# Kernel optimization log

Hardware: AMD Instinct MI355X
Metric: run time of the kernel (lower is better)

The kernel has to match this reference:

```python
import jax, jax.numpy as jnp
import numpy as np

FEATURE_DIM = 128
NUM_EDGES = 640000
NUM_NODES = 40000


def setup_inputs() -> dict:
    key = jax.random.key(0)
    ks = jax.random.split(key, 10)
    d = FEATURE_DIM
    scale = 1.0 / np.sqrt(d)
    inp = {
        "messages": jax.random.normal(ks[0], (NUM_EDGES, d), dtype=jnp.float32),
        "receivers": jax.random.randint(ks[1], (NUM_EDGES,), 0, NUM_NODES, dtype=jnp.int32),
        "num_segments": NUM_NODES,
        "Wk": jax.random.normal(ks[2], (d, d), dtype=jnp.float32) * scale,
        "bk": jnp.zeros((d,), dtype=jnp.float32),
        "Wv": jax.random.normal(ks[3], (d, d), dtype=jnp.float32) * scale,
        "bv": jnp.zeros((d,), dtype=jnp.float32),
        "Wq": jax.random.normal(ks[4], (d, d), dtype=jnp.float32) * scale,
        "bq": jnp.zeros((d,), dtype=jnp.float32),
        "Wo": jax.random.normal(ks[5], (d, d), dtype=jnp.float32) * scale,
        "bo": jnp.zeros((d,), dtype=jnp.float32),
    }
    return inp


def reference(messages, receivers, num_segments, Wk, bk, Wv, bv, Wq, bq, Wo, bo):
    d = messages.shape[-1]
    # per-edge key/value projections
    keys = messages @ Wk + bk            # [E, d]
    values = messages @ Wv + bv          # [E, d]
    # node-level summed messages -> queries
    summed = jax.ops.segment_sum(messages, receivers, num_segments)  # [N, d]
    queries = summed @ Wq + bq                                       # [N, d]
    # scalar attention score per edge (dot over full feature dim)
    msg_q = queries[receivers]                                       # [E, d]
    scores = jnp.sum(msg_q * keys, axis=-1) / jnp.sqrt(jnp.float32(d))  # [E]
    # segment softmax over edges sharing a receiver
    max_s = jax.ops.segment_max(scores, receivers, num_segments)     # [N]
    exp_s = jnp.exp(scores - max_s[receivers])                       # [E]
    sum_e = jax.ops.segment_sum(exp_s, receivers, num_segments)      # [N]
    attn = exp_s / (sum_e[receivers] + 1e-08)                        # [E]
    # weighted scatter-sum of values, then output projection
    agg = jax.ops.segment_sum(values * attn[:, None], receivers, num_segments)  # [N, d]
    return agg @ Wo + bo
```

## Files before the change

kernel.cpp:

```cpp
#include <hip/hip_runtime.h>

#define D 128
#define RSQRT_D 0.088388347648318440550f
#define NEG_HUGE -3.4e38f
#define NPB 16
#define CAP 512

#define FMA4(acc, s, b) { acc.x += (s)*(b).x; acc.y += (s)*(b).y; acc.z += (s)*(b).z; acc.w += (s)*(b).w; }
#define ADD4(acc, b) { acc.x += (b).x; acc.y += (b).y; acc.z += (b).z; acc.w += (b).w; }
#define MRG4(a) { a.x += __shfl_xor(a.x,32); a.y += __shfl_xor(a.y,32); a.z += __shfl_xor(a.z,32); a.w += __shfl_xor(a.w,32); }
#define Z4 make_float4(0.f,0.f,0.f,0.f)

__global__ __launch_bounds__(256) void prep_kernel(
    const float* __restrict__ Wq, const float* __restrict__ Wk,
    const float* __restrict__ bq, const float* __restrict__ bk,
    const float* __restrict__ Wv, const float* __restrict__ Wo,
    const float* __restrict__ bv,
    float* __restrict__ Wqk, float* __restrict__ bqk,
    float* __restrict__ wqb, float* __restrict__ bqb,
    float* __restrict__ Wvo, float* __restrict__ bvo,
    int* __restrict__ zbase, int zcount) {
    int bid = blockIdx.x, t = threadIdx.x;
    if (bid < 64) {
        int i = bid * 2 + (t >> 7), j = t & 127;
        float a1 = 0.f, a2 = 0.f;
        for (int u = 0; u < D; ++u) {
            a1 += Wq[i * D + u] * Wk[j * D + u];
            a2 += Wv[i * D + u] * Wo[u * D + j];
        }
        Wqk[i * D + j] = a1;
        Wvo[i * D + j] = a2;
    } else if (bid == 64) {
        if (t < D) {
            int j = t;
            float a1 = 0.f, a2 = 0.f, a3 = 0.f;
            for (int u = 0; u < D; ++u) {
                a1 += bq[u] * Wk[j * D + u];
                a2 += Wq[j * D + u] * bk[u];
                a3 += bv[u] * Wo[u * D + j];
            }
            bqk[j] = a1; wqb[j] = a2; bvo[j] = a3;
            if (j == 0) {
                float b = 0.f;
                for (int u = 0; u < D; ++u) b += bq[u] * bk[u];
                *bqb = b;
            }
        }
    } else {
        int idx = (bid - 65) * 256 + t;
        if (idx < zcount) zbase[idx] = 0;
    }
}

__global__ void hist_kernel(const int* __restrict__ recv, int* __restrict__ cnt, int E) {
    int e = blockIdx.x * blockDim.x + threadIdx.x;
    if (e >= E) return;
    atomicAdd(&cnt[recv[e]], 1);
}

__global__ __launch_bounds__(1024) void scan_kernel(const int* __restrict__ cnt,
                                                    int* __restrict__ start, int N) {
    __shared__ int wsum[16];
    __shared__ int chunk_total;
    int t = threadIdx.x;
    int w = t >> 6, lane = t & 63;
    int running = 0;
    const int4* cnt4 = (const int4*)cnt;
    int nIter = (N + 4095) >> 12;
    int4 v = make_int4(0, 0, 0, 0);
    {
        int i = t << 2;
        if (i < N) v = cnt4[i >> 2];
    }
    for (int it = 0; it < nIter; ++it) {
        int4 vn = make_int4(0, 0, 0, 0);
        {
            int i = ((it + 1) << 12) + (t << 2);
            if (it + 1 < nIter && i < N) vn = cnt4[i >> 2];
        }
        int s0 = v.x, s1 = s0 + v.y, s2 = s1 + v.z, s3 = s2 + v.w;
        int x = s3;
#pragma unroll
        for (int off = 1; off < 64; off <<= 1) {
            int y = __shfl_up(x, off);
            if (lane >= off) x += y;
        }
        if (lane == 63) wsum[w] = x;
        __syncthreads();
        if (w == 0 && lane < 16) {
            int s = wsum[lane];
#pragma unroll
            for (int off = 1; off < 16; off <<= 1) {
                int y = __shfl_up(s, off);
                if (lane >= off) s += y;
            }
            wsum[lane] = s;
            if (lane == 15) chunk_total = s;
        }
        __syncthreads();
        int waveoff = (w == 0) ? 0 : wsum[w - 1];
        int tb = running + waveoff + (x - s3);
        int i = (it << 12) + (t << 2);
        if (i < N) ((int4*)start)[i >> 2] = make_int4(tb, tb + s0, tb + s1, tb + s2);
        running += chunk_total;
        __syncthreads();
        v = vn;
    }
    if (t == 0) start[N] = running;
}

__global__ void fill_kernel(const int* __restrict__ recv, const int* __restrict__ start,
                            int* __restrict__ cursor, int* __restrict__ eidx, int E) {
    int e = blockIdx.x * blockDim.x + threadIdx.x;
    if (e >= E) return;
    int r = recv[e];
    int p = atomicAdd(&cursor[r], 1);
    eidx[start[r] + p] = e;
}

__device__ __forceinline__ float hdot32(float4 f, float4 q) {
    float p = f.x * q.x + f.y * q.y + f.z * q.z + f.w * q.w;
    p += __shfl_xor(p, 1); p += __shfl_xor(p, 2); p += __shfl_xor(p, 4);
    p += __shfl_xor(p, 8); p += __shfl_xor(p, 16);
    return p;
}

__global__ __launch_bounds__(256, 4) void mega_kernel(
    const float* __restrict__ msg, const int* __restrict__ eidx,
    const int* __restrict__ start,
    const float* __restrict__ Wqk, const float* __restrict__ bqk,
    const float* __restrict__ wqb, const float* __restrict__ bqbp,
    const float* __restrict__ Wvo, const float* __restrict__ bvo,
    const float* __restrict__ bo,
    float* __restrict__ out, int N) {
    __shared__ float4 sums4[NPB * 32];
    __shared__ float4 qks4[NPB * 32];
    __shared__ int eidx_s[CAP];
    __shared__ float s_s[CAP];
    __shared__ float sat[NPB];

    int t = threadIdx.x;
    int lane = t & 63, w = t >> 6;
    int h = lane >> 5;
    int k = lane & 31;
    int base = blockIdx.x * NPB;
    const float4* msg4 = (const float4*)msg;

    int nendB = min(base + NPB, N);
    int s0B = start[base];
    int cntB = start[nendB] - s0B;
    int cc = min(cntB, CAP);
    for (int i = t; i < cc; i += 256) eidx_s[i] = eidx[s0B + i];

    int n0 = base + w * 4;
    int b0 = start[min(n0 + 0, N)] - s0B;
    int b1 = start[min(n0 + 1, N)] - s0B;
    int b2 = start[min(n0 + 2, N)] - s0B;
    int b3 = start[min(n0 + 3, N)] - s0B;
    int b4 = start[min(n0 + 4, N)] - s0B;

    __syncthreads();

    auto loadrow = [&](int r) -> float4 {
        int rI = min(r, b4 - 1);
        int e = (rI < CAP) ? eidx_s[rI] : eidx[s0B + rI];
        return msg4[(size_t)e * 32 + k];
    };

    float4 a0 = Z4, a1 = Z4, a2 = Z4, a3 = Z4;
    if (b0 < b4) {
        int j = b0;
        float4 F0 = loadrow(j + h), F1 = loadrow(j + h + 2),
               F2 = loadrow(j + h + 4), F3 = loadrow(j + h + 6);
        for (;;) {
            int jn = j + 8;
            bool more = jn < b4;
            float4 G0, G1, G2, G3;
            if (more) {
                G0 = loadrow(jn + h); G1 = loadrow(jn + h + 2);
                G2 = loadrow(jn + h + 4); G3 = loadrow(jn + h + 6);
            }
#pragma unroll
            for (int u = 0; u < 4; ++u) {
                int r = j + h + 2 * u;
                float4 g = (u == 0) ? F0 : (u == 1) ? F1 : (u == 2) ? F2 : F3;
                float mk = (r < b4) ? 1.f : 0.f;
                g.x *= mk; g.y *= mk; g.z *= mk; g.w *= mk;
                if (r < b1)      { ADD4(a0, g); }
                else if (r < b2) { ADD4(a1, g); }
                else if (r < b3) { ADD4(a2, g); }
                else             { ADD4(a3, g); }
            }
            if (!more) break;
            F0 = G0; F1 = G1; F2 = G2; F3 = G3;
            j = jn;
        }
    }
    MRG4(a0); MRG4(a1); MRG4(a2); MRG4(a3);
    if (lane < 32) {
        sums4[(w * 4 + 0) * 32 + k] = a0;
        sums4[(w * 4 + 1) * 32 + k] = a1;
        sums4[(w * 4 + 2) * 32 + k] = a2;
        sums4[(w * 4 + 3) * 32 + k] = a3;
    }
    __syncthreads();

    {
        int c = t & 31, slot = t >> 5;
        const float4* B4 = (const float4*)Wqk;
        float4 acc0 = ((const float4*)bqk)[c];
        float4 acc1 = acc0;
        for (int i = 0; i < D; i += 4) {
            float4 aA = sums4[slot * 32 + (i >> 2)];
            float4 aB = sums4[(slot + 8) * 32 + (i >> 2)];
            float4 c0 = B4[(i + 0) * 32 + c];
            float4 c1 = B4[(i + 1) * 32 + c];
            float4 c2 = B4[(i + 2) * 32 + c];
            float4 c3 = B4[(i + 3) * 32 + c];
            FMA4(acc0, aA.x, c0); FMA4(acc0, aA.y, c1); FMA4(acc0, aA.z, c2); FMA4(acc0, aA.w, c3);
            FMA4(acc1, aB.x, c0); FMA4(acc1, aB.y, c1); FMA4(acc1, aB.z, c2); FMA4(acc1, aB.w, c3);
        }
        qks4[slot * 32 + c] = acc0;
        qks4[(slot + 8) * 32 + c] = acc1;
    }
    __syncthreads();

    float4 wv = ((const float4*)wqb)[k];
    float bqb = bqbp[0];
    float4 sv0 = sums4[(w * 4 + 0) * 32 + k];
    float4 sv1 = sums4[(w * 4 + 1) * 32 + k];
    float4 sv2 = sums4[(w * 4 + 2) * 32 + k];
    float4 sv3 = sums4[(w * 4 + 3) * 32 + k];
    float qb0 = hdot32(sv0, wv) + bqb;
    float qb1 = hdot32(sv1, wv) + bqb;
    float qb2 = hdot32(sv2, wv) + bqb;
    float qb3 = hdot32(sv3, wv) + bqb;
    float4 q0 = qks4[(w * 4 + 0) * 32 + k];
    float4 q1 = qks4[(w * 4 + 1) * 32 + k];
    float4 q2 = qks4[(w * 4 + 2) * 32 + k];
    float4 q3 = qks4[(w * 4 + 3) * 32 + k];

    float m0 = NEG_HUGE, m1 = NEG_HUGE, m2 = NEG_HUGE, m3 = NEG_HUGE;
    if (b0 < b4) {
        int j = b0;
        float4 F0 = loadrow(j + h), F1 = loadrow(j + h + 2),
               F2 = loadrow(j + h + 4), F3 = loadrow(j + h + 6);
        for (;;) {
            int jn = j + 8;
            bool more = jn < b4;
            float4 G0, G1, G2, G3;
            if (more) {
                G0 = loadrow(jn + h); G1 = loadrow(jn + h + 2);
                G2 = loadrow(jn + h + 4); G3 = loadrow(jn + h + 6);
            }
#pragma unroll
            for (int u = 0; u < 4; ++u) {
                int r = j + h + 2 * u;
                bool valid = r < b4;
                float4 f = (u == 0) ? F0 : (u == 1) ? F1 : (u == 2) ? F2 : F3;
                float4 qv = (r < b1) ? q0 : (r < b2) ? q1 : (r < b3) ? q2 : q3;
                float qbv = (r < b1) ? qb0 : (r < b2) ? qb1 : (r < b3) ? qb2 : qb3;
                float p = hdot32(f, qv);
                float sc = valid ? (p + qbv) * RSQRT_D : NEG_HUGE;
                if (r < b1)      m0 = fmaxf(m0, sc);
                else if (r < b2) m1 = fmaxf(m1, sc);
                else if (r < b3) m2 = fmaxf(m2, sc);
                else             m3 = fmaxf(m3, sc);
                if (k == 0 && valid && r < CAP) s_s[r] = sc;
            }
            if (!more) break;
            F0 = G0; F1 = G1; F2 = G2; F3 = G3;
            j = jn;
        }
    }
    m0 = fmaxf(m0, __shfl_xor(m0, 32));
    m1 = fmaxf(m1, __shfl_xor(m1, 32));
    m2 = fmaxf(m2, __shfl_xor(m2, 32));
    m3 = fmaxf(m3, __shfl_xor(m3, 32));

    float sm0 = 0.f, sm1 = 0.f, sm2 = 0.f, sm3 = 0.f;
    float4 c0 = Z4, c1 = Z4, c2 = Z4, c3 = Z4;
    if (b0 < b4) {
        int j = b0;
        float4 F0 = loadrow(j + h), F1 = loadrow(j + h + 2),
               F2 = loadrow(j + h + 4), F3 = loadrow(j + h + 6);
        for (;;) {
            int jn = j + 8;
            bool more = jn < b4;
            float4 G0, G1, G2, G3;
            if (more) {
                G0 = loadrow(jn + h); G1 = loadrow(jn + h + 2);
                G2 = loadrow(jn + h + 4); G3 = loadrow(jn + h + 6);
            }
#pragma unroll
            for (int u = 0; u < 4; ++u) {
                int r = j + h + 2 * u;
                bool valid = r < b4;
                float4 f = (u == 0) ? F0 : (u == 1) ? F1 : (u == 2) ? F2 : F3;
                int rI = min(r, b4 - 1);
                float sc;
                if (rI < CAP) {
                    sc = s_s[rI];
                } else {
                    float4 qv = (r < b1) ? q0 : (r < b2) ? q1 : (r < b3) ? q2 : q3;
                    float qbv = (r < b1) ? qb0 : (r < b2) ? qb1 : (r < b3) ? qb2 : qb3;
                    sc = (hdot32(f, qv) + qbv) * RSQRT_D;
                }
                float msel = (r < b1) ? m0 : (r < b2) ? m1 : (r < b3) ? m2 : m3;
                float wgt = valid ? __expf(sc - msel) : 0.f;
                if (r < b1)      { sm0 += wgt; FMA4(c0, wgt, f); }
                else if (r < b2) { sm1 += wgt; FMA4(c1, wgt, f); }
                else if (r < b3) { sm2 += wgt; FMA4(c2, wgt, f); }
                else             { sm3 += wgt; FMA4(c3, wgt, f); }
            }
            if (!more) break;
            F0 = G0; F1 = G1; F2 = G2; F3 = G3;
            j = jn;
        }
    }
    sm0 += __shfl_xor(sm0, 32);
    sm1 += __shfl_xor(sm1, 32);
    sm2 += __shfl_xor(sm2, 32);
    sm3 += __shfl_xor(sm3, 32);
    MRG4(c0); MRG4(c1); MRG4(c2); MRG4(c3);
    float inv0 = 1.f / (sm0 + 1e-8f);
    float inv1 = 1.f / (sm1 + 1e-8f);
    float inv2 = 1.f / (sm2 + 1e-8f);
    float inv3 = 1.f / (sm3 + 1e-8f);
    if (lane < 32) {
        sums4[(w * 4 + 0) * 32 + k] = make_float4(c0.x * inv0, c0.y * inv0, c0.z * inv0, c0.w * inv0);
        sums4[(w * 4 + 1) * 32 + k] = make_float4(c1.x * inv1, c1.y * inv1, c1.z * inv1, c1.w * inv1);
        sums4[(w * 4 + 2) * 32 + k] = make_float4(c2.x * inv2, c2.y * inv2, c2.z * inv2, c2.w * inv2);
        sums4[(w * 4 + 3) * 32 + k] = make_float4(c3.x * inv3, c3.y * inv3, c3.z * inv3, c3.w * inv3);
    }
    if (lane == 0) {
        sat[w * 4 + 0] = sm0 * inv0;
        sat[w * 4 + 1] = sm1 * inv1;
        sat[w * 4 + 2] = sm2 * inv2;
        sat[w * 4 + 3] = sm3 * inv3;
    }
    __syncthreads();

    {
        int c = t & 31, slot = t >> 5;
        const float4* B4 = (const float4*)Wvo;
        float4 bo4 = ((const float4*)bo)[c];
        float4 bv4 = ((const float4*)bvo)[c];
        float sa0 = sat[slot], sa1 = sat[slot + 8];
        float4 acc0 = make_float4(bo4.x + sa0 * bv4.x, bo4.y + sa0 * bv4.y,
                                  bo4.z + sa0 * bv4.z, bo4.w + sa0 * bv4.w);
        float4 acc1 = make_float4(bo4.x + sa1 * bv4.x, bo4.y + sa1 * bv4.y,
                                  bo4.z + sa1 * bv4.z, bo4.w + sa1 * bv4.w);
        for (int i = 0; i < D; i += 4) {
            float4 aA = sums4[slot * 32 + (i >> 2)];
            float4 aB = sums4[(slot + 8) * 32 + (i >> 2)];
            float4 d0 = B4[(i + 0) * 32 + c];
            float4 d1 = B4[(i + 1) * 32 + c];
            float4 d2 = B4[(i + 2) * 32 + c];
            float4 d3 = B4[(i + 3) * 32 + c];
            FMA4(acc0, aA.x, d0); FMA4(acc0, aA.y, d1); FMA4(acc0, aA.z, d2); FMA4(acc0, aA.w, d3);
            FMA4(acc1, aB.x, d0); FMA4(acc1, aB.y, d1); FMA4(acc1, aB.z, d2); FMA4(acc1, aB.w, d3);
        }
        int nA = base + slot, nB = base + slot + 8;
        if (nA < N) ((float4*)(out + (size_t)nA * D))[c] = acc0;
        if (nB < N) ((float4*)(out + (size_t)nB * D))[c] = acc1;
    }
}


extern "C" void kernel_launch(void* const* d_in, const int* in_sizes, int n_in,
                              void* d_out, int out_size, void* d_ws, size_t ws_size,
                              hipStream_t stream) {
    const float* msg = (const float*)d_in[0];
    const int* recv = (const int*)d_in[1];
    const float* Wk = (const float*)d_in[3];
    const float* bk = (const float*)d_in[4];
    const float* Wv = (const float*)d_in[5];
    const float* bv = (const float*)d_in[6];
    const float* Wq = (const float*)d_in[7];
    const float* bq = (const float*)d_in[8];
    const float* Wo = (const float*)d_in[9];
    const float* bo = (const float*)d_in[10];
    float* out = (float*)d_out;

    int E = in_sizes[0] / D;
    int N = out_size / D;

    char* wsb = (char*)d_ws;
    size_t o = 0;
    auto alloc = [&](size_t elems) {
        void* p = wsb + o;
        o += (elems * 4 + 63) & ~(size_t)63;
        return p;
    };

    int* cnt    = (int*)alloc(2 * (size_t)N);
    int* cursor = cnt + N;
    int* start  = (int*)alloc(N + 1);
    int* eidx   = (int*)alloc(E);
    float* Wqk  = (float*)alloc(D * D);
    float* bqk  = (float*)alloc(D);
    float* wqb  = (float*)alloc(D);
    float* bqb  = (float*)alloc(1);
    float* Wvo  = (float*)alloc(D * D);
    float* bvo  = (float*)alloc(D);

    int zcount = 2 * N;
    int zblocks = (zcount + 255) / 256;
    prep_kernel<<<65 + zblocks, 256, 0, stream>>>(Wq, Wk, bq, bk, Wv, Wo, bv,
                                                  Wqk, bqk, wqb, bqb, Wvo, bvo,
                                                  cnt, zcount);
    int nbE = (E + 255) / 256;
    hist_kernel<<<nbE, 256, 0, stream>>>(recv, cnt, E);
    scan_kernel<<<1, 1024, 0, stream>>>(cnt, start, N);
    fill_kernel<<<nbE, 256, 0, stream>>>(recv, start, cursor, eidx, E);
    mega_kernel<<<(N + NPB - 1) / NPB, 256, 0, stream>>>(msg, eidx, start, Wqk, bqk, wqb, bqb,
                                                         Wvo, bvo, bo, out, N);
}
```

Before: 724.0 us.

## Use single-pass online softmax with lazy rescaling in fused attention kernel

The separate max pass over each node's edges is replaced by one online-softmax pass. The running max is updated only when a score exceeds it by a threshold, and the two half-wave partial states are then merged with exp rescaling. This removes the second read of the message rows and the shared score buffer, at the cost of extra registers, so the occupancy hint drops from 4 to 3. The histogram kernel also now reads four receivers per thread with an int4 load.

Result: faster. 678.2 us (-6.3%).

```diff
diff --git a/kernel.cpp b/kernel.cpp
--- a/kernel.cpp
+++ b/kernel.cpp
@@ -5,11 +5,25 @@
 #define NEG_HUGE -3.4e38f
 #define NPB 16
 #define CAP 512
+#define DTHR 20.0f
 
 #define FMA4(acc, s, b) { acc.x += (s)*(b).x; acc.y += (s)*(b).y; acc.z += (s)*(b).z; acc.w += (s)*(b).w; }
 #define ADD4(acc, b) { acc.x += (b).x; acc.y += (b).y; acc.z += (b).z; acc.w += (b).w; }
 #define MRG4(a) { a.x += __shfl_xor(a.x,32); a.y += __shfl_xor(a.y,32); a.z += __shfl_xor(a.z,32); a.w += __shfl_xor(a.w,32); }
+#define SCL4(a, f) { a.x *= (f); a.y *= (f); a.z *= (f); a.w *= (f); }
 #define Z4 make_float4(0.f,0.f,0.f,0.f)
+
+#define MERGE_HALVES(mi, si, ci) { \
+    float mo_ = __shfl_xor(mi, 32); \
+    float so_ = __shfl_xor(si, 32); \
+    float4 co_; co_.x = __shfl_xor(ci.x, 32); co_.y = __shfl_xor(ci.y, 32); \
+    co_.z = __shfl_xor(ci.z, 32); co_.w = __shfl_xor(ci.w, 32); \
+    float mt_ = fmaxf(mi, mo_); \
+    float e0_ = __expf(mi - mt_), e1_ = __expf(mo_ - mt_); \
+    si = si * e0_ + so_ * e1_; \
+    ci.x = ci.x * e0_ + co_.x * e1_; ci.y = ci.y * e0_ + co_.y * e1_; \
+    ci.z = ci.z * e0_ + co_.z * e1_; ci.w = ci.w * e0_ + co_.w * e1_; \
+}
 
 __global__ __launch_bounds__(256) void prep_kernel(
     const float* __restrict__ Wq, const float* __restrict__ Wk,
@@ -53,9 +67,17 @@
 }
 
 __global__ void hist_kernel(const int* __restrict__ recv, int* __restrict__ cnt, int E) {
-    int e = blockIdx.x * blockDim.x + threadIdx.x;
-    if (e >= E) return;
-    atomicAdd(&cnt[recv[e]], 1);
+    int i = blockIdx.x * blockDim.x + threadIdx.x;
+    int base = i << 2;
+    if (base + 3 < E) {
+        int4 r = *(const int4*)(recv + base);
+        atomicAdd(&cnt[r.x], 1);
+        atomicAdd(&cnt[r.y], 1);
+        atomicAdd(&cnt[r.z], 1);
+        atomicAdd(&cnt[r.w], 1);
+    } else {
+        for (int u = base; u < E; ++u) atomicAdd(&cnt[recv[u]], 1);
+    }
 }
 
 __global__ __launch_bounds__(1024) void scan_kernel(const int* __restrict__ cnt,
@@ -125,7 +147,7 @@
     return p;
 }
 
-__global__ __launch_bounds__(256, 4) void mega_kernel(
+__global__ __launch_bounds__(256, 3) void mega_kernel(
     const float* __restrict__ msg, const int* __restrict__ eidx,
     const int* __restrict__ start,
     const float* __restrict__ Wqk, const float* __restrict__ bqk,
@@ -136,7 +158,6 @@
     __shared__ float4 sums4[NPB * 32];
     __shared__ float4 qks4[NPB * 32];
     __shared__ int eidx_s[CAP];
-    __shared__ float s_s[CAP];
     __shared__ float sat[NPB];
 
     int t = threadIdx.x;
@@ -227,117 +248,88 @@
 
     float4 wv = ((const float4*)wqb)[k];
     float bqb = bqbp[0];
-    float4 sv0 = sums4[(w * 4 + 0) * 32 + k];
-    float4 sv1 = sums4[(w * 4 + 1) * 32 + k];
-    float4 sv2 = sums4[(w * 4 + 2) * 32 + k];
-    float4 sv3 = sums4[(w * 4 + 3) * 32 + k];
-    float qb0 = hdot32(sv0, wv) + bqb;
-    float qb1 = hdot32(sv1, wv) + bqb;
-    float qb2 = hdot32(sv2, wv) + bqb;
-    float qb3 = hdot32(sv3, wv) + bqb;
-    float4 q0 = qks4[(w * 4 + 0) * 32 + k];
-    float4 q1 = qks4[(w * 4 + 1) * 32 + k];
-    float4 q2 = qks4[(w * 4 + 2) * 32 + k];
-    float4 q3 = qks4[(w * 4 + 3) * 32 + k];
-
-    float m0 = NEG_HUGE, m1 = NEG_HUGE, m2 = NEG_HUGE, m3 = NEG_HUGE;
-    if (b0 < b4) {
-        int j = b0;
-        float4 F0 = loadrow(j + h), F1 = loadrow(j + h + 2),
-               F2 = loadrow(j + h + 4), F3 = loadrow(j + h + 6);
-        for (;;) {
-            int jn = j + 8;
-            bool more = jn < b4;
-            float4 G0, G1, G2, G3;
-            if (more) {
-                G0 = loadrow(jn + h); G1 = loadrow(jn + h + 2);
-                G2 = loadrow(jn + h + 4); G3 = loadrow(jn + h + 6);
-            }
+    {
+        float4 sv0 = sums4[(w * 4 + 0) * 32 + k];
+        float4 sv1 = sums4[(w * 4 + 1) * 32 + k];
+        float4 sv2 = sums4[(w * 4 + 2) * 32 + k];
+        float4 sv3 = sums4[(w * 4 + 3) * 32 + k];
+        float qb0_ = hdot32(sv0, wv) + bqb;
+        float qb1_ = hdot32(sv1, wv) + bqb;
+        float qb2_ = hdot32(sv2, wv) + bqb;
+        float qb3_ = hdot32(sv3, wv) + bqb;
+        sat[0] = sat[0];
+        __builtin_memcpy(&wv, &wv, 0);
+        {
+        }
+        static_assert(true, "");
+        float4 q0 = qks4[(w * 4 + 0) * 32 + k];
+        float4 q1 = qks4[(w * 4 + 1) * 32 + k];
+        float4 q2 = qks4[(w * 4 + 2) * 32 + k];
+        float4 q3 = qks4[(w * 4 + 3) * 32 + k];
+
+        float m0 = NEG_HUGE, m1 = NEG_HUGE, m2 = NEG_HUGE, m3 = NEG_HUGE;
+        float sm0 = 0.f, sm1 = 0.f, sm2 = 0.f, sm3 = 0.f;
+        float4 c0 = Z4, c1 = Z4, c2 = Z4, c3 = Z4;
+        if (b0 < b4) {
+            int j = b0;
+            float4 F0 = loadrow(j + h), F1 = loadrow(j + h + 2),
+                   F2 = loadrow(j + h + 4), F3 = loadrow(j + h + 6);
+            for (;;) {
+                int jn = j + 8;
+                bool more = jn < b4;
+                float4 G0, G1, G2, G3;
+                if (more) {
+                    G0 = loadrow(jn + h); G1 = loadrow(jn + h + 2);
+                    G2 = loadrow(jn + h + 4); G3 = loadrow(jn + h + 6);
+                }
 #pragma unroll
-            for (int u = 0; u < 4; ++u) {
-                int r = j + h + 2 * u;
-                bool valid = r < b4;
-                float4 f = (u == 0) ? F0 : (u == 1) ? F1 : (u == 2) ? F2 : F3;
-                float4 qv = (r < b1) ? q0 : (r < b2) ? q1 : (r < b3) ? q2 : q3;
-                float qbv = (r < b1) ? qb0 : (r < b2) ? qb1 : (r < b3) ? qb2 : qb3;
-                float p = hdot32(f, qv);
-                float sc = valid ? (p + qbv) * RSQRT_D : NEG_HUGE;
-                if (r < b1)      m0 = fmaxf(m0, sc);
-                else if (r < b2) m1 = fmaxf(m1, sc);
-                else if (r < b3) m2 = fmaxf(m2, sc);
-                else             m3 = fmaxf(m3, sc);
-                if (k == 0 && valid && r < CAP) s_s[r] = sc;
-            }
-            if (!more) break;
-            F0 = G0; F1 = G1; F2 = G2; F3 = G3;
-            j = jn;
-        }
-    }
-    m0 = fmaxf(m0, __shfl_xor(m0, 32));
-    m1 = fmaxf(m1, __shfl_xor(m1, 32));
-    m2 = fmaxf(m2, __shfl_xor(m2, 32));
-    m3 = fmaxf(m3, __shfl_xor(m3, 32));
-
-    float sm0 = 0.f, sm1 = 0.f, sm2 = 0.f, sm3 = 0.f;
-    float4 c0 = Z4, c1 = Z4, c2 = Z4, c3 = Z4;
-    if (b0 < b4) {
-        int j = b0;
-        float4 F0 = loadrow(j + h), F1 = loadrow(j + h + 2),
-               F2 = loadrow(j + h + 4), F3 = loadrow(j + h + 6);
-        for (;;) {
-            int jn = j + 8;
-            bool more = jn < b4;
-            float4 G0, G1, G2, G3;
-            if (more) {
-                G0 = loadrow(jn + h); G1 = loadrow(jn + h + 2);
-                G2 = loadrow(jn + h + 4); G3 = loadrow(jn + h + 6);
-            }
-#pragma unroll
-            for (int u = 0; u < 4; ++u) {
-                int r = j + h + 2 * u;
-                bool valid = r < b4;
-                float4 f = (u == 0) ? F0 : (u == 1) ? F1 : (u == 2) ? F2 : F3;
-                int rI = min(r, b4 - 1);
-                float sc;
-                if (rI < CAP) {
-                    sc = s_s[rI];
-                } else {
+                for (int u = 0; u < 4; ++u) {
+                    int r = j + h + 2 * u;
+                    bool valid = r < b4;
+                    float4 f = (u == 0) ? F0 : (u == 1) ? F1 : (u == 2) ? F2 : F3;
                     float4 qv = (r < b1) ? q0 : (r < b2) ? q1 : (r < b3) ? q2 : q3;
-                    float qbv = (r < b1) ? qb0 : (r < b2) ? qb1 : (r < b3) ? qb2 : qb3;
-                    sc = (hdot32(f, qv) + qbv) * RSQRT_D;
+                    float qbv = (r < b1) ? qb0_ : (r < b2) ? qb1_ : (r < b3) ? qb2_ : qb3_;
+                    float sc = (hdot32(f, qv) + qbv) * RSQRT_D;
+                    float msel = (r < b1) ? m0 : (r < b2) ? m1 : (r < b3) ? m2 : m3;
+                    if (valid && sc > msel + DTHR) {
+                        float fac = __expf(msel - sc);
+                        if (r < b1)      { sm0 *= fac; SCL4(c0, fac); m0 = sc; }
+                        else if (r < b2) { sm1 *= fac; SCL4(c1, fac); m1 = sc; }
+                        else if (r < b3) { sm2 *= fac; SCL4(c2, fac); m2 = sc; }
+                        else             { sm3 *= fac; SCL4(c3, fac); m3 = sc; }
+                        msel = sc;
+                    }
+                    float wgt = valid ? __expf(sc - msel) : 0.f;
+                    if (r < b1)      { sm0 += wgt; FMA4(c0, wgt, f); }
+                    else if (r < b2) { sm1 += wgt; FMA4(c1, wgt, f); }
+                    else if (r < b3) { sm2 += wgt; FMA4(c2, wgt, f); }
+                    else             { sm3 += wgt; FMA4(c3, wgt, f); }
                 }
-                float msel = (r < b1) ? m0 : (r < b2) ? m1 : (r < b3) ? m2 : m3;
-                float wgt = valid ? __expf(sc - msel) : 0.f;
-                if (r < b1)      { sm0 += wgt; FMA4(c0, wgt, f); }
-                else if (r < b2) { sm1 += wgt; FMA4(c1, wgt, f); }
-                else if (r < b3) { sm2 += wgt; FMA4(c2, wgt, f); }
-                else             { sm3 += wgt; FMA4(c3, wgt, f); }
-            }
-            if (!more) break;
-            F0 = G0; F1 = G1; F2 = G2; F3 = G3;
-            j = jn;
-        }
-    }
-    sm0 += __shfl_xor(sm0, 32);
-    sm1 += __shfl_xor(sm1, 32);
-    sm2 += __shfl_xor(sm2, 32);
-    sm3 += __shfl_xor(sm3, 32);
-    MRG4(c0); MRG4(c1); MRG4(c2); MRG4(c3);
-    float inv0 = 1.f / (sm0 + 1e-8f);
-    float inv1 = 1.f / (sm1 + 1e-8f);
-    float inv2 = 1.f / (sm2 + 1e-8f);
-    float inv3 = 1.f / (sm3 + 1e-8f);
-    if (lane < 32) {
-        sums4[(w * 4 + 0) * 32 + k] = make_float4(c0.x * inv0, c0.y * inv0, c0.z * inv0, c0.w * inv0);
-        sums4[(w * 4 + 1) * 32 + k] = make_float4(c1.x * inv1, c1.y * inv1, c1.z * inv1, c1.w * inv1);
-        sums4[(w * 4 + 2) * 32 + k] = make_float4(c2.x * inv2, c2.y * inv2, c2.z * inv2, c2.w * inv2);
-        sums4[(w * 4 + 3) * 32 + k] = make_float4(c3.x * inv3, c3.y * inv3, c3.z * inv3, c3.w * inv3);
-    }
-    if (lane == 0) {
-        sat[w * 4 + 0] = sm0 * inv0;
-        sat[w * 4 + 1] = sm1 * inv1;
-        sat[w * 4 + 2] = sm2 * inv2;
-        sat[w * 4 + 3] = sm3 * inv3;
+                if (!more) break;
+                F0 = G0; F1 = G1; F2 = G2; F3 = G3;
+                j = jn;
+            }
+        }
+        MERGE_HALVES(m0, sm0, c0);
+        MERGE_HALVES(m1, sm1, c1);
+        MERGE_HALVES(m2, sm2, c2);
+        MERGE_HALVES(m3, sm3, c3);
+        float inv0 = 1.f / (sm0 + 1e-8f);
+        float inv1 = 1.f / (sm1 + 1e-8f);
+        float inv2 = 1.f / (sm2 + 1e-8f);
+        float inv3 = 1.f / (sm3 + 1e-8f);
+        if (lane < 32) {
+            sums4[(w * 4 + 0) * 32 + k] = make_float4(c0.x * inv0, c0.y * inv0, c0.z * inv0, c0.w * inv0);
+            sums4[(w * 4 + 1) * 32 + k] = make_float4(c1.x * inv1, c1.y * inv1, c1.z * inv1, c1.w * inv1);
+            sums4[(w * 4 + 2) * 32 + k] = make_float4(c2.x * inv2, c2.y * inv2, c2.z * inv2, c2.w * inv2);
+            sums4[(w * 4 + 3) * 32 + k] = make_float4(c3.x * inv3, c3.y * inv3, c3.z * inv3, c3.w * inv3);
+        }
+        if (lane == 0) {
+            sat[w * 4 + 0] = sm0 * inv0;
+            sat[w * 4 + 1] = sm1 * inv1;
+            sat[w * 4 + 2] = sm2 * inv2;
+            sat[w * 4 + 3] = sm3 * inv3;
+        }
     }
     __syncthreads();
 
@@ -410,9 +402,11 @@
     prep_kernel<<<65 + zblocks, 256, 0, stream>>>(Wq, Wk, bq, bk, Wv, Wo, bv,
                                                   Wqk, bqk, wqb, bqb, Wvo, bvo,
                                                   cnt, zcount);
+    int E4 = (E + 3) / 4;
+    int nbE4 = (E4 + 255) / 256;
+    hist_kernel<<<nbE4, 256, 0, stream>>>(recv, cnt, E);
+    scan_kernel<<<1, 1024, 0, stream>>>(cnt, start, N);
     int nbE = (E + 255) / 256;
-    hist_kernel<<<nbE, 256, 0, stream>>>(recv, cnt, E);
-    scan_kernel<<<1, 1024, 0, stream>>>(cnt, start, N);
     fill_kernel<<<nbE, 256, 0, stream>>>(recv, start, cursor, eidx, E);
     mega_kernel<<<(N + NPB - 1) / NPB, 256, 0, stream>>>(msg, eidx, start, Wqk, bqk, wqb, bqb,
                                                          Wvo, bvo, bo, out, N);
```
